# Kernel tuning notes

Measured on AMD Instinct MI355X. Metric: run time of the kernel, lower is better.

Reference implementation:

```python
import jax, jax.numpy as jnp
import numpy as np

N = 50000   # nodes (cells)
E = 800000  # directed edges
D = 512     # input/output feature dim (genes)
H = D // 64 # bottleneck dim = 8
LN_EPS = 1e-5


def setup_inputs() -> dict:
    key = jax.random.key(0)
    ks = jax.random.split(key, 6)
    x = jax.random.normal(ks[0], (N, D), dtype=jnp.float32)
    edge_index = jax.random.randint(ks[1], (2, E), 0, N, dtype=jnp.int64)
    size_factors = jax.random.uniform(ks[2], (N, 1), dtype=jnp.float32) + 0.5
    s1 = float(1.0 / np.sqrt(D))
    W1 = jax.random.uniform(ks[3], (D, H), jnp.float32, -s1, s1)
    b1 = jnp.zeros((H,), jnp.float32)
    gamma = jnp.ones((H,), jnp.float32)
    beta = jnp.zeros((H,), jnp.float32)
    s2 = float(1.0 / np.sqrt(H))
    W2 = jax.random.uniform(ks[4], (H, D), jnp.float32, -s2, s2)
    b2 = jnp.zeros((D,), jnp.float32)
    return {"x": x, "size_factors": size_factors, "W1": W1, "b1": b1,
            "gamma": gamma, "beta": beta, "W2": W2, "b2": b2,
            "edge_index": edge_index}


def _gcn_conv(x, W, b, src, dst, norm):
    # PyG GCNConv: linear transform, then sym-normalized scatter-add aggregation.
    h = x @ W                                   # [N, out]
    msg = h[src] * norm[:, None]                # [E+N, out] gather + scale
    out = jax.ops.segment_sum(msg, dst, num_segments=N)  # scatter-add
    return out + b


def reference(x, size_factors, W1, b1, gamma, beta, W2, b2, edge_index):
    loops = jnp.arange(N, dtype=edge_index.dtype)
    src = jnp.concatenate([edge_index[0], loops])  # add self-loops
    dst = jnp.concatenate([edge_index[1], loops])
    deg = jax.ops.segment_sum(jnp.ones_like(src, dtype=x.dtype), dst,
                              num_segments=N)       # deg >= 1 via self-loops
    dinv = jax.lax.rsqrt(deg)
    norm = dinv[src] * dinv[dst]                    # [E+N]

    h = _gcn_conv(x, W1, b1, src, dst, norm)        # [N, H]
    mu = jnp.mean(h, axis=-1, keepdims=True)
    var = jnp.var(h, axis=-1, keepdims=True)
    h = (h - mu) * jax.lax.rsqrt(var + LN_EPS) * gamma + beta
    h = jax.nn.relu(h)
    # dropout p=0.0 -> identity
    out = jax.nn.relu(_gcn_conv(h, W2, b2, src, dst, norm))  # [N, D]
    return out * size_factors
```

## Files before the change

### kernel.cpp

```cpp
#include <hip/hip_runtime.h>

#define NN 50000
#define EE 800000
#define DD 512
#define HH 8
#define BA 160
#define CHUNK 5000
#define NBIN 196
#define BCAP 4608
#define GBLK 782
#define NTILE 3125
#define AGBLK 1563
#define SCANT 192

typedef short bf16x8 __attribute__((ext_vector_type(8)));
typedef float f32x4 __attribute__((ext_vector_type(4)));

union U16 { uint4 u; bf16x8 v; unsigned short h[8]; };

__device__ __forceinline__ unsigned short f2bf(float f) {
    union { float f; unsigned int i; } c; c.f = f;
    unsigned int i = c.i;
    i += 0x7fffu + ((i >> 16) & 1u);
    return (unsigned short)(i >> 16);
}

__global__ __launch_bounds__(256) void k_gemm1_hist(const float4* __restrict__ x4,
                                                    const float* __restrict__ W1,
                                                    const int* __restrict__ dst,
                                                    float* __restrict__ t1,
                                                    int* __restrict__ blockhist) {
    __shared__ int smem[4096];
    int t = threadIdx.x;
    if (blockIdx.x >= GBLK) {
        int blk = blockIdx.x - GBLK;
        int* h = smem;
        h[t] = 0; __syncthreads();
        int base = blk * CHUNK;
#pragma unroll
        for (int it = 0; it < 20; ++it) {
            int i = it * 256 + t;
            if (i < CHUNK) atomicAdd(&h[dst[base + i] >> 8], 1);
        }
        __syncthreads();
        blockhist[blk * 256 + t] = h[t];
        return;
    }
    unsigned short* sbf = (unsigned short*)smem;
    for (int i = t; i < 16 * 64 * 8; i += 256) {
        int lane = (i >> 3) & 63, j = i & 7;
        int n = lane & 15;
        int k = (i >> 9) * 32 + ((lane >> 4) * 8) + j;
        sbf[i] = (n < HH) ? f2bf(W1[k * HH + n]) : (unsigned short)0;
    }
    __syncthreads();
    int wave = t >> 6, lane = t & 63;
    int tile = blockIdx.x * 4 + wave;
    if (tile >= NTILE) return;
    int node0 = tile * 16;
    int m = lane & 15, q = lane >> 4;
    const float4* xrow = x4 + (size_t)(node0 + m) * (DD / 4) + q * 2;
    const uint4* bfrag = (const uint4*)sbf;
    f32x4 acc = {0.f, 0.f, 0.f, 0.f};

    float4 bufA[8], bufB[8];
#define LOADG(buf, g)                                                      \
    _Pragma("unroll")                                                      \
    for (int s = 0; s < 4; ++s) {                                          \
        buf[2 * s]     = xrow[((g) * 4 + s) * 8];                          \
        buf[2 * s + 1] = xrow[((g) * 4 + s) * 8 + 1];                      \
    }
#define MFMAG(buf, g)                                                      \
    _Pragma("unroll")                                                      \
    for (int s = 0; s < 4; ++s) {                                          \
        U16 a, b;                                                          \
        float4 u0 = buf[2 * s], u1 = buf[2 * s + 1];                       \
        a.h[0] = f2bf(u0.x); a.h[1] = f2bf(u0.y);                          \
        a.h[2] = f2bf(u0.z); a.h[3] = f2bf(u0.w);                          \
        a.h[4] = f2bf(u1.x); a.h[5] = f2bf(u1.y);                          \
        a.h[6] = f2bf(u1.z); a.h[7] = f2bf(u1.w);                          \
        b.u = bfrag[((g) * 4 + s) * 64 + lane];                            \
        acc = __builtin_amdgcn_mfma_f32_16x16x32_bf16(a.v, b.v, acc, 0, 0, 0); \
    }
    LOADG(bufA, 0)
    LOADG(bufB, 1)
    MFMAG(bufA, 0)
    LOADG(bufA, 2)
    MFMAG(bufB, 1)
    LOADG(bufB, 3)
    MFMAG(bufA, 2)
    MFMAG(bufB, 3)
#undef LOADG
#undef MFMAG
    if (m < HH) {
        int base = (node0 + q * 4) * HH + m;
        t1[base]          = acc[0];
        t1[base + HH]     = acc[1];
        t1[base + 2 * HH] = acc[2];
        t1[base + 3 * HH] = acc[3];
    }
}

__global__ __launch_bounds__(SCANT) void k_scan_a(int* __restrict__ blockhist,
                                                  int* __restrict__ binTotal) {
    __shared__ int s[SCANT];
    int bin = blockIdx.x, t = threadIdx.x;
    int v = (t < BA) ? blockhist[t * 256 + bin] : 0;
    s[t] = v; __syncthreads();
    for (int off = 1; off < SCANT; off <<= 1) {
        int x = (t >= off) ? s[t - off] : 0;
        __syncthreads();
        if (t >= off) s[t] += x;
        __syncthreads();
    }
    if (t < BA) blockhist[t * 256 + bin] = s[t] - v;
    if (t == SCANT - 1) binTotal[bin] = s[t];
}

__global__ __launch_bounds__(256) void k_scan_b(const int* __restrict__ binTotal,
                                                int* __restrict__ binBase,
                                                int* __restrict__ row) {
    __shared__ int s[256];
    int t = threadIdx.x;
    int v = binTotal[t];
    s[t] = v; __syncthreads();
    for (int off = 1; off < 256; off <<= 1) {
        int x = (t >= off) ? s[t - off] : 0;
        __syncthreads();
        if (t >= off) s[t] += x;
        __syncthreads();
    }
    binBase[t] = s[t] - v;
    if (t == 255) { binBase[256] = s[255]; row[NN] = s[255]; }
}

__global__ __launch_bounds__(256) void k_scatter(const int* __restrict__ eidx,
                                                 const int* __restrict__ blockhist,
                                                 const int* __restrict__ binBase,
                                                 int* __restrict__ bucket) {
    __shared__ int cur[256];
    int t = threadIdx.x, blk = blockIdx.x;
    cur[t] = binBase[t] + blockhist[blk * 256 + t]; __syncthreads();
    int base = blk * CHUNK;
#pragma unroll
    for (int it = 0; it < 20; ++it) {
        int i = it * 256 + t;
        if (i < CHUNK) {
            int s = eidx[base + i], d = eidx[EE + base + i];
            int pos = atomicAdd(&cur[d >> 8], 1);
            bucket[pos] = (s << 8) | (d & 255);
        }
    }
}

__global__ __launch_bounds__(256) void k_build(const int* __restrict__ bucket,
                                               const int* __restrict__ binBase,
                                               int* __restrict__ row,
                                               int* __restrict__ adj,
                                               float* __restrict__ dinvA) {
    __shared__ int smem[2 * BCAP + 768];
    int t = threadIdx.x;
    int bin = blockIdx.x;
    int n0 = bin << 8;
    int segStart = binBase[bin];
    int count = binBase[bin + 1] - segStart;
    if (count > BCAP) count = BCAP;
    int* lds_in  = smem;
    int* lds_out = smem + BCAP;
    int* cnt     = smem + 2 * BCAP;
    int* off     = smem + 2 * BCAP + 256;
    int* cur2    = smem + 2 * BCAP + 512;
    cnt[t] = 0; __syncthreads();
    for (int i = t; i < count; i += 256) {
        int p = bucket[segStart + i];
        lds_in[i] = p;
        atomicAdd(&cnt[p & 255], 1);
    }
    __syncthreads();
    off[t] = cnt[t]; __syncthreads();
    for (int o = 1; o < 256; o <<= 1) {
        int x = (t >= o) ? off[t - o] : 0;
        __syncthreads();
        if (t >= o) off[t] += x;
        __syncthreads();
    }
    int excl = off[t] - cnt[t];
    cur2[t] = excl;
    int n = n0 + t;
    if (n < NN) {
        row[n] = segStart + excl;
        dinvA[n] = rsqrtf((float)cnt[t] + 1.0f);
    }
    __syncthreads();
    for (int i = t; i < count; i += 256) {
        int p = lds_in[i];
        int pos = atomicAdd(&cur2[p & 255], 1);
        lds_out[pos] = p >> 8;
    }
    __syncthreads();
    for (int i = t; i < count; i += 256)
        adj[segStart + i] = lds_out[i];
}

__global__ __launch_bounds__(256) void k_agg1(const float* __restrict__ t1,
                                              const int* __restrict__ row,
                                              const int* __restrict__ adj,
                                              const float* __restrict__ dinvA,
                                              const float* __restrict__ b1,
                                              const float* __restrict__ gma,
                                              const float* __restrict__ bta,
                                              float* __restrict__ h2) {
    int gid = blockIdx.x * 256 + threadIdx.x;
    int n = gid >> 3, f = gid & 7;
    if (n >= NN) return;
    int beg = row[n], end = row[n + 1];
    float dv = dinvA[n];
    float acc = t1[(size_t)n * HH + f] * dv;
    int i = beg;
    for (; i + 4 <= end; i += 4) {
        int s0 = adj[i], s1 = adj[i + 1], s2 = adj[i + 2], s3 = adj[i + 3];
        float w0 = dinvA[s0], w1 = dinvA[s1], w2 = dinvA[s2], w3 = dinvA[s3];
        float v0 = t1[(size_t)s0 * HH + f], v1 = t1[(size_t)s1 * HH + f];
        float v2 = t1[(size_t)s2 * HH + f], v3 = t1[(size_t)s3 * HH + f];
        acc += v0 * w0 + v1 * w1 + v2 * w2 + v3 * w3;
    }
    for (; i < end; ++i) {
        int s0 = adj[i];
        acc += t1[(size_t)s0 * HH + f] * dinvA[s0];
    }
    acc = acc * dv + b1[f];
    float s = acc;
    s += __shfl_xor(s, 1); s += __shfl_xor(s, 2); s += __shfl_xor(s, 4);
    float mu = s * 0.125f;
    float dx = acc - mu;
    float sq = dx * dx;
    sq += __shfl_xor(sq, 1); sq += __shfl_xor(sq, 2); sq += __shfl_xor(sq, 4);
    float rs = rsqrtf(sq * 0.125f + 1e-5f);
    h2[(size_t)n * HH + f] = fmaxf(dx * rs * gma[f] + bta[f], 0.f);
}

__global__ __launch_bounds__(256) void k_agg2_gemm2(const float* __restrict__ h2,
                                                    const int* __restrict__ row,
                                                    const int* __restrict__ adj,
                                                    const float* __restrict__ dinvA,
                                                    const float* __restrict__ W2,
                                                    const float* __restrict__ b2,
                                                    const float* __restrict__ sf,
                                                    float* __restrict__ out) {
    __shared__ float sA[32 * 8];
    int tid = threadIdx.x;
    int c = tid & 63, g = tid >> 6, d0 = c * 8;
    float w[8][8];
#pragma unroll
    for (int k = 0; k < 8; ++k) {
        float4 u0 = *(const float4*)(W2 + k * DD + d0);
        float4 u1 = *(const float4*)(W2 + k * DD + d0 + 4);
        w[k][0] = u0.x; w[k][1] = u0.y; w[k][2] = u0.z; w[k][3] = u0.w;
        w[k][4] = u1.x; w[k][5] = u1.y; w[k][6] = u1.z; w[k][7] = u1.w;
    }
    float bb[8];
    {
        float4 u0 = *(const float4*)(b2 + d0);
        float4 u1 = *(const float4*)(b2 + d0 + 4);
        bb[0] = u0.x; bb[1] = u0.y; bb[2] = u0.z; bb[3] = u0.w;
        bb[4] = u1.x; bb[5] = u1.y; bb[6] = u1.z; bb[7] = u1.w;
    }
    int nl = tid >> 3, f = tid & 7;
    int n = blockIdx.x * 32 + nl;
    if (n < NN) {
        int beg = row[n], end = row[n + 1];
        float dv = dinvA[n];
        float acc = h2[(size_t)n * HH + f] * dv;
        int i = beg;
        for (; i + 4 <= end; i += 4) {
            int s0 = adj[i], s1 = adj[i + 1], s2 = adj[i + 2], s3 = adj[i + 3];
            float w0 = dinvA[s0], w1 = dinvA[s1], w2 = dinvA[s2], w3 = dinvA[s3];
            float v0 = h2[(size_t)s0 * HH + f], v1 = h2[(size_t)s1 * HH + f];
            float v2 = h2[(size_t)s2 * HH + f], v3 = h2[(size_t)s3 * HH + f];
            acc += v0 * w0 + v1 * w1 + v2 * w2 + v3 * w3;
        }
        for (; i < end; ++i) {
            int s0 = adj[i];
            acc += h2[(size_t)s0 * HH + f] * dinvA[s0];
        }
        sA[nl * 8 + f] = acc * dv;
    }
    __syncthreads();
#pragma unroll
    for (int i = 0; i < 8; ++i) {
        int rrow = i * 4 + g;
        int n2 = blockIdx.x * 32 + rrow;
        if (n2 < NN) {
            float a[8];
#pragma unroll
            for (int j = 0; j < 8; ++j) a[j] = sA[rrow * 8 + j];
            float s = sf[n2];
            float acc[8];
#pragma unroll
            for (int j = 0; j < 8; ++j) acc[j] = bb[j];
#pragma unroll
            for (int k = 0; k < 8; ++k)
#pragma unroll
                for (int j = 0; j < 8; ++j) acc[j] += a[k] * w[k][j];
            float4 o0 = make_float4(fmaxf(acc[0], 0.f) * s, fmaxf(acc[1], 0.f) * s,
                                    fmaxf(acc[2], 0.f) * s, fmaxf(acc[3], 0.f) * s);
            float4 o1 = make_float4(fmaxf(acc[4], 0.f) * s, fmaxf(acc[5], 0.f) * s,
                                    fmaxf(acc[6], 0.f) * s, fmaxf(acc[7], 0.f) * s);
            float4* op = (float4*)(out + (size_t)n2 * DD + d0);
            op[0] = o0;
            op[1] = o1;
        }
    }
}

extern "C" void kernel_launch(void* const* d_in, const int* in_sizes, int n_in,
                              void* d_out, int out_size, void* d_ws, size_t ws_size,
                              hipStream_t stream) {
    (void)in_sizes; (void)n_in; (void)out_size; (void)ws_size;
    const float* x   = (const float*)d_in[0];
    const float* sf  = (const float*)d_in[1];
    const float* W1  = (const float*)d_in[2];
    const float* b1  = (const float*)d_in[3];
    const float* gma = (const float*)d_in[4];
    const float* bta = (const float*)d_in[5];
    const float* W2  = (const float*)d_in[6];
    const float* b2  = (const float*)d_in[7];
    const int* eidx  = (const int*)d_in[8];
    float* out = (float*)d_out;

    char* ws = (char*)d_ws;
    int*   blockhist = (int*)(ws + 0);
    int*   binBase   = (int*)(ws + 262144);
    int*   binTotal  = (int*)(ws + 262144 + 2048);
    int*   row       = (int*)(ws + (1 << 20));
    float* dinvA     = (float*)(ws + 2 * (1 << 20));
    float* t1        = (float*)(ws + 3 * (1 << 20));
    float* h2        = (float*)(ws + 5 * (1 << 20));
    int*   adj       = (int*)(ws + 7 * (1 << 20));
    int*   bucket    = (int*)(ws + 11 * (1 << 20));

    k_gemm1_hist<<<GBLK + BA, 256, 0, stream>>>((const float4*)x, W1, eidx + EE,
                                                t1, blockhist);
    k_scan_a<<<256, SCANT, 0, stream>>>(blockhist, binTotal);
    k_scan_b<<<1, 256, 0, stream>>>(binTotal, binBase, row);
    k_scatter<<<BA, 256, 0, stream>>>(eidx, blockhist, binBase, bucket);
    k_build<<<NBIN, 256, 0, stream>>>(bucket, binBase, row, adj, dinvA);
    k_agg1<<<AGBLK, 256, 0, stream>>>(t1, row, adj, dinvA, b1, gma, bta, h2);
    k_agg2_gemm2<<<AGBLK, 256, 0, stream>>>(h2, row, adj, dinvA, W2, b2, sf, out);
}
```

Measured before the change: 273.7 us.

## Fuse CSR build stages and GEMM1 into one kernel with grid barriers

Merges the histogram, two scans, scatter and per-bin build kernels into a single launch. The first 256 blocks run the CSR construction and synchronise through atomic-counter grid barriers, while the remaining blocks do the first GEMM concurrently. This removes four kernel launches and their inter-kernel gaps and lets the GEMM overlap with the CSR phases. The trade-offs are a memset on every call and spin-wait barriers, which depend on all 256 barrier blocks being co-resident and could deadlock if the GEMM blocks get scheduled ahead of them.

```diff
diff --git a/kernel.cpp b/kernel.cpp
--- a/kernel.cpp
+++ b/kernel.cpp
@@ -11,7 +11,8 @@
 #define GBLK 782
 #define NTILE 3125
 #define AGBLK 1563
-#define SCANT 192
+#define GOFF 256
+#define CSRB 256
 
 typedef short bf16x8 __attribute__((ext_vector_type(8)));
 typedef float f32x4 __attribute__((ext_vector_type(4)));
@@ -25,45 +26,52 @@
     return (unsigned short)(i >> 16);
 }
 
-__global__ __launch_bounds__(256) void k_gemm1_hist(const float4* __restrict__ x4,
-                                                    const float* __restrict__ W1,
-                                                    const int* __restrict__ dst,
-                                                    float* __restrict__ t1,
-                                                    int* __restrict__ blockhist) {
-    __shared__ int smem[4096];
+__device__ __forceinline__ void gbar(int* c) {
+    __syncthreads();
+    if (threadIdx.x == 0) {
+        __hip_atomic_fetch_add(c, 1, __ATOMIC_ACQ_REL, __HIP_MEMORY_SCOPE_AGENT);
+        while (__hip_atomic_load(c, __ATOMIC_ACQUIRE, __HIP_MEMORY_SCOPE_AGENT) < CSRB)
+            __builtin_amdgcn_s_sleep(1);
+    }
+    __syncthreads();
+}
+
+__global__ __launch_bounds__(256) void k_mega(const float4* __restrict__ x4,
+                                              const float* __restrict__ W1,
+                                              const int* __restrict__ eidx,
+                                              float* __restrict__ t1,
+                                              int* __restrict__ blockhist,
+                                              int* __restrict__ binTotal,
+                                              int* __restrict__ binBase,
+                                              int* __restrict__ bucket,
+                                              int* __restrict__ row,
+                                              int* __restrict__ adj,
+                                              float* __restrict__ dinvA,
+                                              int* __restrict__ bar) {
+    __shared__ int smem[2 * BCAP + 768];
     int t = threadIdx.x;
-    if (blockIdx.x >= GBLK) {
-        int blk = blockIdx.x - GBLK;
-        int* h = smem;
-        h[t] = 0; __syncthreads();
-        int base = blk * CHUNK;
-#pragma unroll
-        for (int it = 0; it < 20; ++it) {
-            int i = it * 256 + t;
-            if (i < CHUNK) atomicAdd(&h[dst[base + i] >> 8], 1);
-        }
-        __syncthreads();
-        blockhist[blk * 256 + t] = h[t];
-        return;
-    }
-    unsigned short* sbf = (unsigned short*)smem;
-    for (int i = t; i < 16 * 64 * 8; i += 256) {
-        int lane = (i >> 3) & 63, j = i & 7;
-        int n = lane & 15;
-        int k = (i >> 9) * 32 + ((lane >> 4) * 8) + j;
-        sbf[i] = (n < HH) ? f2bf(W1[k * HH + n]) : (unsigned short)0;
-    }
-    __syncthreads();
-    int wave = t >> 6, lane = t & 63;
-    int tile = blockIdx.x * 4 + wave;
-    if (tile >= NTILE) return;
-    int node0 = tile * 16;
-    int m = lane & 15, q = lane >> 4;
-    const float4* xrow = x4 + (size_t)(node0 + m) * (DD / 4) + q * 2;
-    const uint4* bfrag = (const uint4*)sbf;
-    f32x4 acc = {0.f, 0.f, 0.f, 0.f};
-
-    float4 bufA[8], bufB[8];
+    int b = blockIdx.x;
+    const int* dst = eidx + EE;
+
+    if (b >= GOFF) {
+        unsigned short* sbf = (unsigned short*)smem;
+        for (int i = t; i < 16 * 64 * 8; i += 256) {
+            int lane = (i >> 3) & 63, j = i & 7;
+            int n = lane & 15;
+            int k = (i >> 9) * 32 + ((lane >> 4) * 8) + j;
+            sbf[i] = (n < HH) ? f2bf(W1[k * HH + n]) : (unsigned short)0;
+        }
+        __syncthreads();
+        int wave = t >> 6, lane = t & 63;
+        int tile = (b - GOFF) * 4 + wave;
+        if (tile >= NTILE) return;
+        int node0 = tile * 16;
+        int m = lane & 15, q = lane >> 4;
+        const float4* xrow = x4 + (size_t)(node0 + m) * (DD / 4) + q * 2;
+        const uint4* bfrag = (const uint4*)sbf;
+        f32x4 acc = {0.f, 0.f, 0.f, 0.f};
+
+        float4 bufA[8], bufB[8];
 #define LOADG(buf, g)                                                      \
     _Pragma("unroll")                                                      \
     for (int s = 0; s < 4; ++s) {                                          \
@@ -73,133 +81,138 @@
 #define MFMAG(buf, g)                                                      \
     _Pragma("unroll")                                                      \
     for (int s = 0; s < 4; ++s) {                                          \
-        U16 a, b;                                                          \
+        U16 a, bb;                                                         \
         float4 u0 = buf[2 * s], u1 = buf[2 * s + 1];                       \
         a.h[0] = f2bf(u0.x); a.h[1] = f2bf(u0.y);                          \
         a.h[2] = f2bf(u0.z); a.h[3] = f2bf(u0.w);                          \
         a.h[4] = f2bf(u1.x); a.h[5] = f2bf(u1.y);                          \
         a.h[6] = f2bf(u1.z); a.h[7] = f2bf(u1.w);                          \
-        b.u = bfrag[((g) * 4 + s) * 64 + lane];                            \
-        acc = __builtin_amdgcn_mfma_f32_16x16x32_bf16(a.v, b.v, acc, 0, 0, 0); \
-    }
-    LOADG(bufA, 0)
-    LOADG(bufB, 1)
-    MFMAG(bufA, 0)
-    LOADG(bufA, 2)
-    MFMAG(bufB, 1)
-    LOADG(bufB, 3)
-    MFMAG(bufA, 2)
-    MFMAG(bufB, 3)
+        bb.u = bfrag[((g) * 4 + s) * 64 + lane];                           \
+        acc = __builtin_amdgcn_mfma_f32_16x16x32_bf16(a.v, bb.v, acc, 0, 0, 0); \
+    }
+        LOADG(bufA, 0)
+        LOADG(bufB, 1)
+        MFMAG(bufA, 0)
+        LOADG(bufA, 2)
+        MFMAG(bufB, 1)
+        LOADG(bufB, 3)
+        MFMAG(bufA, 2)
+        MFMAG(bufB, 3)
 #undef LOADG
 #undef MFMAG
-    if (m < HH) {
-        int base = (node0 + q * 4) * HH + m;
-        t1[base]          = acc[0];
-        t1[base + HH]     = acc[1];
-        t1[base + 2 * HH] = acc[2];
-        t1[base + 3 * HH] = acc[3];
-    }
-}
-
-__global__ __launch_bounds__(SCANT) void k_scan_a(int* __restrict__ blockhist,
-                                                  int* __restrict__ binTotal) {
-    __shared__ int s[SCANT];
-    int bin = blockIdx.x, t = threadIdx.x;
-    int v = (t < BA) ? blockhist[t * 256 + bin] : 0;
-    s[t] = v; __syncthreads();
-    for (int off = 1; off < SCANT; off <<= 1) {
-        int x = (t >= off) ? s[t - off] : 0;
-        __syncthreads();
-        if (t >= off) s[t] += x;
-        __syncthreads();
-    }
-    if (t < BA) blockhist[t * 256 + bin] = s[t] - v;
-    if (t == SCANT - 1) binTotal[bin] = s[t];
-}
-
-__global__ __launch_bounds__(256) void k_scan_b(const int* __restrict__ binTotal,
-                                                int* __restrict__ binBase,
-                                                int* __restrict__ row) {
-    __shared__ int s[256];
-    int t = threadIdx.x;
-    int v = binTotal[t];
-    s[t] = v; __syncthreads();
-    for (int off = 1; off < 256; off <<= 1) {
-        int x = (t >= off) ? s[t - off] : 0;
-        __syncthreads();
-        if (t >= off) s[t] += x;
-        __syncthreads();
-    }
-    binBase[t] = s[t] - v;
-    if (t == 255) { binBase[256] = s[255]; row[NN] = s[255]; }
-}
-
-__global__ __launch_bounds__(256) void k_scatter(const int* __restrict__ eidx,
-                                                 const int* __restrict__ blockhist,
-                                                 const int* __restrict__ binBase,
-                                                 int* __restrict__ bucket) {
-    __shared__ int cur[256];
-    int t = threadIdx.x, blk = blockIdx.x;
-    cur[t] = binBase[t] + blockhist[blk * 256 + t]; __syncthreads();
-    int base = blk * CHUNK;
-#pragma unroll
-    for (int it = 0; it < 20; ++it) {
-        int i = it * 256 + t;
-        if (i < CHUNK) {
-            int s = eidx[base + i], d = eidx[EE + base + i];
-            int pos = atomicAdd(&cur[d >> 8], 1);
-            bucket[pos] = (s << 8) | (d & 255);
-        }
-    }
-}
-
-__global__ __launch_bounds__(256) void k_build(const int* __restrict__ bucket,
-                                               const int* __restrict__ binBase,
-                                               int* __restrict__ row,
-                                               int* __restrict__ adj,
-                                               float* __restrict__ dinvA) {
-    __shared__ int smem[2 * BCAP + 768];
-    int t = threadIdx.x;
-    int bin = blockIdx.x;
-    int n0 = bin << 8;
-    int segStart = binBase[bin];
-    int count = binBase[bin + 1] - segStart;
-    if (count > BCAP) count = BCAP;
-    int* lds_in  = smem;
-    int* lds_out = smem + BCAP;
-    int* cnt     = smem + 2 * BCAP;
-    int* off     = smem + 2 * BCAP + 256;
-    int* cur2    = smem + 2 * BCAP + 512;
-    cnt[t] = 0; __syncthreads();
-    for (int i = t; i < count; i += 256) {
-        int p = bucket[segStart + i];
-        lds_in[i] = p;
-        atomicAdd(&cnt[p & 255], 1);
-    }
-    __syncthreads();
-    off[t] = cnt[t]; __syncthreads();
-    for (int o = 1; o < 256; o <<= 1) {
-        int x = (t >= o) ? off[t - o] : 0;
-        __syncthreads();
-        if (t >= o) off[t] += x;
-        __syncthreads();
-    }
-    int excl = off[t] - cnt[t];
-    cur2[t] = excl;
-    int n = n0 + t;
-    if (n < NN) {
-        row[n] = segStart + excl;
-        dinvA[n] = rsqrtf((float)cnt[t] + 1.0f);
-    }
-    __syncthreads();
-    for (int i = t; i < count; i += 256) {
-        int p = lds_in[i];
-        int pos = atomicAdd(&cur2[p & 255], 1);
-        lds_out[pos] = p >> 8;
-    }
-    __syncthreads();
-    for (int i = t; i < count; i += 256)
-        adj[segStart + i] = lds_out[i];
+        if (m < HH) {
+            int base = (node0 + q * 4) * HH + m;
+            t1[base]          = acc[0];
+            t1[base + HH]     = acc[1];
+            t1[base + 2 * HH] = acc[2];
+            t1[base + 3 * HH] = acc[3];
+        }
+        return;
+    }
+
+    if (b < BA) {
+        int* h = smem;
+        h[t] = 0; __syncthreads();
+        int base = b * CHUNK;
+#pragma unroll
+        for (int it = 0; it < 20; ++it) {
+            int i = it * 256 + t;
+            if (i < CHUNK) atomicAdd(&h[dst[base + i] >> 8], 1);
+        }
+        __syncthreads();
+        blockhist[b * 256 + t] = h[t];
+    }
+    gbar(bar + 0);
+
+    {
+        int* s = smem;
+        int v = (t < BA) ? blockhist[t * 256 + b] : 0;
+        s[t] = v; __syncthreads();
+        for (int off = 1; off < 256; off <<= 1) {
+            int x = (t >= off) ? s[t - off] : 0;
+            __syncthreads();
+            if (t >= off) s[t] += x;
+            __syncthreads();
+        }
+        if (t < BA) blockhist[t * 256 + b] = s[t] - v;
+        if (t == 255) binTotal[b] = s[255];
+    }
+    gbar(bar + 1);
+
+    if (b == 0) {
+        int* s = smem;
+        int v = binTotal[t];
+        s[t] = v; __syncthreads();
+        for (int off = 1; off < 256; off <<= 1) {
+            int x = (t >= off) ? s[t - off] : 0;
+            __syncthreads();
+            if (t >= off) s[t] += x;
+            __syncthreads();
+        }
+        binBase[t] = s[t] - v;
+        if (t == 255) { binBase[256] = s[255]; row[NN] = s[255]; }
+    }
+    gbar(bar + 2);
+
+    if (b < BA) {
+        int* cur = smem;
+        cur[t] = binBase[t] + blockhist[b * 256 + t];
+        __syncthreads();
+        int base = b * CHUNK;
+#pragma unroll
+        for (int it = 0; it < 20; ++it) {
+            int i = it * 256 + t;
+            if (i < CHUNK) {
+                int s_ = eidx[base + i], d = eidx[EE + base + i];
+                int pos = atomicAdd(&cur[d >> 8], 1);
+                bucket[pos] = (s_ << 8) | (d & 255);
+            }
+        }
+    }
+    gbar(bar + 3);
+
+    if (b < NBIN) {
+        int bin = b;
+        int n0 = bin << 8;
+        int segStart = binBase[bin];
+        int count = binBase[bin + 1] - segStart;
+        if (count > BCAP) count = BCAP;
+        int* lds_in  = smem;
+        int* lds_out = smem + BCAP;
+        int* cnt     = smem + 2 * BCAP;
+        int* off     = smem + 2 * BCAP + 256;
+        int* cur2    = smem + 2 * BCAP + 512;
+        cnt[t] = 0; __syncthreads();
+        for (int i = t; i < count; i += 256) {
+            int p = bucket[segStart + i];
+            lds_in[i] = p;
+            atomicAdd(&cnt[p & 255], 1);
+        }
+        __syncthreads();
+        off[t] = cnt[t]; __syncthreads();
+        for (int o = 1; o < 256; o <<= 1) {
+            int x = (t >= o) ? off[t - o] : 0;
+            __syncthreads();
+            if (t >= o) off[t] += x;
+            __syncthreads();
+        }
+        int excl = off[t] - cnt[t];
+        cur2[t] = excl;
+        int n = n0 + t;
+        if (n < NN) {
+            row[n] = segStart + excl;
+            dinvA[n] = rsqrtf((float)cnt[t] + 1.0f);
+        }
+        __syncthreads();
+        for (int i = t; i < count; i += 256) {
+            int p = lds_in[i];
+            int pos = atomicAdd(&cur2[p & 255], 1);
+            lds_out[pos] = p >> 8;
+        }
+        __syncthreads();
+        for (int i = t; i < count; i += 256)
+            adj[segStart + i] = lds_out[i];
+    }
 }
 
 __global__ __launch_bounds__(256) void k_agg1(const float* __restrict__ t1,
@@ -332,6 +345,7 @@
     int*   blockhist = (int*)(ws + 0);
     int*   binBase   = (int*)(ws + 262144);
     int*   binTotal  = (int*)(ws + 262144 + 2048);
+    int*   bar       = (int*)(ws + 262144 + 4096);
     int*   row       = (int*)(ws + (1 << 20));
     float* dinvA     = (float*)(ws + 2 * (1 << 20));
     float* t1        = (float*)(ws + 3 * (1 << 20));
@@ -339,12 +353,10 @@
     int*   adj       = (int*)(ws + 7 * (1 << 20));
     int*   bucket    = (int*)(ws + 11 * (1 << 20));
 
-    k_gemm1_hist<<<GBLK + BA, 256, 0, stream>>>((const float4*)x, W1, eidx + EE,
-                                                t1, blockhist);
-    k_scan_a<<<256, SCANT, 0, stream>>>(blockhist, binTotal);
-    k_scan_b<<<1, 256, 0, stream>>>(binTotal, binBase, row);
-    k_scatter<<<BA, 256, 0, stream>>>(eidx, blockhist, binBase, bucket);
-    k_build<<<NBIN, 256, 0, stream>>>(bucket, binBase, row, adj, dinvA);
+    hipMemsetAsync(bar, 0, 16, stream);
+    k_mega<<<GOFF + GBLK, 256, 0, stream>>>((const float4*)x, W1, eidx, t1,
+                                            blockhist, binTotal, binBase,
+                                            bucket, row, adj, dinvA, bar);
     k_agg1<<<AGBLK, 256, 0, stream>>>(t1, row, adj, dinvA, b1, gma, bta, h2);
     k_agg2_gemm2<<<AGBLK, 256, 0, stream>>>(h2, row, adj, dinvA, W2, b2, sf, out);
 }
```

After: 375.7 us. 37.3% more time.

## Prescale node features by dinv to drop per-edge dinv gathers

Applied to the files above, without the earlier changes.

Folds the source-side normalisation into the node features. t1 is multiplied by dinv in k_build, and h2 is written already scaled by dinv in k_agg1. Both aggregation loops then only gather features, not dinvA[src], and they read adjacency with aligned int4 loads, eight edges per iteration. This halves the random gathers per edge, at the cost of an extra read-modify-write of t1 in k_build and a slightly different floating-point summation order.

```diff
diff --git a/kernel.cpp b/kernel.cpp
--- a/kernel.cpp
+++ b/kernel.cpp
@@ -157,7 +157,8 @@
                                                const int* __restrict__ binBase,
                                                int* __restrict__ row,
                                                int* __restrict__ adj,
-                                               float* __restrict__ dinvA) {
+                                               float* __restrict__ dinvA,
+                                               float* __restrict__ t1) {
     __shared__ int smem[2 * BCAP + 768];
     int t = threadIdx.x;
     int bin = blockIdx.x;
@@ -189,7 +190,13 @@
     int n = n0 + t;
     if (n < NN) {
         row[n] = segStart + excl;
-        dinvA[n] = rsqrtf((float)cnt[t] + 1.0f);
+        float dv = rsqrtf((float)cnt[t] + 1.0f);
+        dinvA[n] = dv;
+        float4* tp = (float4*)(t1 + (size_t)n * HH);
+        float4 a = tp[0], b = tp[1];
+        a.x *= dv; a.y *= dv; a.z *= dv; a.w *= dv;
+        b.x *= dv; b.y *= dv; b.z *= dv; b.w *= dv;
+        tp[0] = a; tp[1] = b;
     }
     __syncthreads();
     for (int i = t; i < count; i += 256) {
@@ -215,19 +222,28 @@
     if (n >= NN) return;
     int beg = row[n], end = row[n + 1];
     float dv = dinvA[n];
-    float acc = t1[(size_t)n * HH + f] * dv;
+    float acc = t1[(size_t)n * HH + f];
     int i = beg;
-    for (; i + 4 <= end; i += 4) {
-        int s0 = adj[i], s1 = adj[i + 1], s2 = adj[i + 2], s3 = adj[i + 3];
-        float w0 = dinvA[s0], w1 = dinvA[s1], w2 = dinvA[s2], w3 = dinvA[s3];
-        float v0 = t1[(size_t)s0 * HH + f], v1 = t1[(size_t)s1 * HH + f];
-        float v2 = t1[(size_t)s2 * HH + f], v3 = t1[(size_t)s3 * HH + f];
-        acc += v0 * w0 + v1 * w1 + v2 * w2 + v3 * w3;
-    }
-    for (; i < end; ++i) {
-        int s0 = adj[i];
-        acc += t1[(size_t)s0 * HH + f] * dinvA[s0];
-    }
+    for (; i < end && (i & 3); ++i)
+        acc += t1[(size_t)adj[i] * HH + f];
+    const int4* a4 = (const int4*)adj;
+    for (; i + 8 <= end; i += 8) {
+        int4 e0 = a4[i >> 2], e1 = a4[(i >> 2) + 1];
+        float v0 = t1[(size_t)e0.x * HH + f], v1 = t1[(size_t)e0.y * HH + f];
+        float v2 = t1[(size_t)e0.z * HH + f], v3 = t1[(size_t)e0.w * HH + f];
+        float v4 = t1[(size_t)e1.x * HH + f], v5 = t1[(size_t)e1.y * HH + f];
+        float v6 = t1[(size_t)e1.z * HH + f], v7 = t1[(size_t)e1.w * HH + f];
+        acc += ((v0 + v1) + (v2 + v3)) + ((v4 + v5) + (v6 + v7));
+    }
+    if (i + 4 <= end) {
+        int4 e0 = a4[i >> 2];
+        float v0 = t1[(size_t)e0.x * HH + f], v1 = t1[(size_t)e0.y * HH + f];
+        float v2 = t1[(size_t)e0.z * HH + f], v3 = t1[(size_t)e0.w * HH + f];
+        acc += (v0 + v1) + (v2 + v3);
+        i += 4;
+    }
+    for (; i < end; ++i)
+        acc += t1[(size_t)adj[i] * HH + f];
     acc = acc * dv + b1[f];
     float s = acc;
     s += __shfl_xor(s, 1); s += __shfl_xor(s, 2); s += __shfl_xor(s, 4);
@@ -236,7 +252,7 @@
     float sq = dx * dx;
     sq += __shfl_xor(sq, 1); sq += __shfl_xor(sq, 2); sq += __shfl_xor(sq, 4);
     float rs = rsqrtf(sq * 0.125f + 1e-5f);
-    h2[(size_t)n * HH + f] = fmaxf(dx * rs * gma[f] + bta[f], 0.f);
+    h2[(size_t)n * HH + f] = fmaxf(dx * rs * gma[f] + bta[f], 0.f) * dv;
 }
 
 __global__ __launch_bounds__(256) void k_agg2_gemm2(const float* __restrict__ h2,
@@ -270,19 +286,28 @@
     if (n < NN) {
         int beg = row[n], end = row[n + 1];
         float dv = dinvA[n];
-        float acc = h2[(size_t)n * HH + f] * dv;
+        float acc = h2[(size_t)n * HH + f];
         int i = beg;
-        for (; i + 4 <= end; i += 4) {
-            int s0 = adj[i], s1 = adj[i + 1], s2 = adj[i + 2], s3 = adj[i + 3];
-            float w0 = dinvA[s0], w1 = dinvA[s1], w2 = dinvA[s2], w3 = dinvA[s3];
-            float v0 = h2[(size_t)s0 * HH + f], v1 = h2[(size_t)s1 * HH + f];
-            float v2 = h2[(size_t)s2 * HH + f], v3 = h2[(size_t)s3 * HH + f];
-            acc += v0 * w0 + v1 * w1 + v2 * w2 + v3 * w3;
-        }
-        for (; i < end; ++i) {
-            int s0 = adj[i];
-            acc += h2[(size_t)s0 * HH + f] * dinvA[s0];
-        }
+        for (; i < end && (i & 3); ++i)
+            acc += h2[(size_t)adj[i] * HH + f];
+        const int4* a4 = (const int4*)adj;
+        for (; i + 8 <= end; i += 8) {
+            int4 e0 = a4[i >> 2], e1 = a4[(i >> 2) + 1];
+            float v0 = h2[(size_t)e0.x * HH + f], v1 = h2[(size_t)e0.y * HH + f];
+            float v2 = h2[(size_t)e0.z * HH + f], v3 = h2[(size_t)e0.w * HH + f];
+            float v4 = h2[(size_t)e1.x * HH + f], v5 = h2[(size_t)e1.y * HH + f];
+            float v6 = h2[(size_t)e1.z * HH + f], v7 = h2[(size_t)e1.w * HH + f];
+            acc += ((v0 + v1) + (v2 + v3)) + ((v4 + v5) + (v6 + v7));
+        }
+        if (i + 4 <= end) {
+            int4 e0 = a4[i >> 2];
+            float v0 = h2[(size_t)e0.x * HH + f], v1 = h2[(size_t)e0.y * HH + f];
+            float v2 = h2[(size_t)e0.z * HH + f], v3 = h2[(size_t)e0.w * HH + f];
+            acc += (v0 + v1) + (v2 + v3);
+            i += 4;
+        }
+        for (; i < end; ++i)
+            acc += h2[(size_t)adj[i] * HH + f];
         sA[nl * 8 + f] = acc * dv;
     }
     __syncthreads();
@@ -344,7 +369,7 @@
     k_scan_a<<<256, SCANT, 0, stream>>>(blockhist, binTotal);
     k_scan_b<<<1, 256, 0, stream>>>(binTotal, binBase, row);
     k_scatter<<<BA, 256, 0, stream>>>(eidx, blockhist, binBase, bucket);
-    k_build<<<NBIN, 256, 0, stream>>>(bucket, binBase, row, adj, dinvA);
+    k_build<<<NBIN, 256, 0, stream>>>(bucket, binBase, row, adj, dinvA, t1);
     k_agg1<<<AGBLK, 256, 0, stream>>>(t1, row, adj, dinvA, b1, gma, bta, h2);
     k_agg2_gemm2<<<AGBLK, 256, 0, stream>>>(h2, row, adj, dinvA, W2, b2, sf, out);
 }
```

After: 270.9 us. Within noise of the previous version (-1.0%).
